# Kernel tuning notes

Measured on AMD Instinct MI355X. Metric: run time of the kernel, lower is better.

Reference implementation:

```python
import jax, jax.numpy as jnp
import numpy as np
from jax.scipy.special import logsumexp

S, L = 32768, 512  # seq_len, label_num


def setup_inputs() -> dict:
    key = jax.random.key(0)
    k1, k2, k3 = jax.random.split(key, 3)
    logit = jax.random.normal(k1, (S, L), dtype=jnp.float32)   # emissions [S, L]
    labels = jax.random.randint(k2, (S,), 0, L)                # gold path [S]
    T = jax.random.normal(k3, (L, L), dtype=jnp.float32)       # T[next, prev]
    return {"logit": logit, "labels": labels, "T": T}


def _crf_loss(logit, T, labels):
    # Forward algorithm: alpha_t[j] = logsumexp_i(alpha_{t-1}[i] + T[j, i]) + feat_t[j]
    alpha0 = logit[0]

    def step(alpha, feat):
        new_alpha = logsumexp(alpha[None, :] + T, axis=1) + feat  # [L]
        return new_alpha, None

    alpha_final, _ = jax.lax.scan(step, alpha0, logit[1:])
    log_Z = logsumexp(alpha_final)

    # Gold path score: feat_0[y0] + sum_{t>0} (feat_t[y_t] + T[y_t, y_{t-1}])
    emit = logit[0, labels[0]] + jnp.sum(logit[jnp.arange(1, logit.shape[0]), labels[1:]])
    trans = jnp.sum(T[labels[1:], labels[:-1]])
    gold = emit + trans
    return log_Z - gold


def reference(logit, labels, T):
    return _crf_loss(logit, T, labels)
```

## Files before the change

kernel.cpp:

```cpp
#include <hip/hip_runtime.h>
#include <stdint.h>


#define S_LEN 32768
#define L 512
#define CH 16
#define NCF 2048
#define WGF 128
#define WGB 128
#define LN448 6.104793232f
#define LN2   0.6931471806f

#define OFF_EAF  0
#define OFF_EAB  (256*1024)
#define OFF_G    (512*1024)
#define OFF_H    (OFF_G + 2048*512*2)
#define OFF_LSE  (OFF_H + 2048*512*2)
#define OFF_GOLD (OFF_LSE + 4104*4)

typedef float v4f __attribute__((ext_vector_type(4)));

__device__ __forceinline__ float b2f(unsigned short u){
  return __uint_as_float(((unsigned)u) << 16);
}
__device__ __forceinline__ unsigned short f2b(float x){
  unsigned u = __float_as_uint(x);
  return (unsigned short)((u + 0x7fffu + ((u >> 16) & 1u)) >> 16);
}
__device__ __forceinline__ unsigned char to_fp8(float v){
  int u = __builtin_amdgcn_cvt_pk_fp8_f32(v, v, 0, false);
  return (unsigned char)(u & 0xff);
}

extern "C" __global__ void crf_prep(const float* __restrict__ T,
                                    unsigned char* __restrict__ EAf,
                                    unsigned char* __restrict__ EAb){
  int tid = blockIdx.x*512 + threadIdx.x;
  int r    = tid & 7;
  int lane = (tid >> 3) & 63;
  int kt   = (tid >> 9) & 15;
  int mtw  = tid >> 13;
  int j = (mtw >> 2)*64 + (mtw & 3)*16 + (lane & 15);
  int i = kt*32 + ((lane >> 4) << 3) + r;
  EAf[tid] = to_fp8(2.0f * __expf(T[j*L + i]));
  EAb[tid] = to_fp8(2.0f * __expf(T[i*L + j]));
}

extern "C" __global__ __launch_bounds__(512, 2)
void crf_chunks(const float* __restrict__ logit,
                const unsigned char* __restrict__ EAf,
                const unsigned char* __restrict__ EAb,
                unsigned short* __restrict__ G, unsigned short* __restrict__ H){
  __shared__ __align__(16) unsigned char Pl[2][8192];
  __shared__ float sPart[16][8];

  const int tid  = threadIdx.x;
  const int w    = tid >> 6;
  const int lane = tid & 63;
  const int quad = lane >> 4;
  const int cl   = lane & 15;
  const bool fwd = (blockIdx.x < WGF);
  const int  b   = fwd ? blockIdx.x : (blockIdx.x - WGF);
  const int  cg  = fwd ? (b*16 + cl) : (1 + b*16 + cl);
  const int  cgc = min(cg, NCF-1);
  const bool isc0 = fwd && (cg == 0);
  const int  jrow0 = w*64 + quad*4;

  const long* EA = (const long*)(fwd ? EAf : EAb);
  long eA[4][16];
  #pragma unroll
  for (int mt = 0; mt < 4; ++mt)
    #pragma unroll
    for (int kt = 0; kt < 16; ++kt)
      eA[mt][kt] = EA[(((w<<2)+mt)<<4 | kt)*64 + lane];

  float vr[4][4];
  if (fwd) {
    #pragma unroll
    for (int mt = 0; mt < 4; ++mt)
      #pragma unroll
      for (int r = 0; r < 4; ++r) vr[mt][r] = 1.0f;
  } else {
    const int t0 = cgc*CH + CH - 1;
    const float* lp = logit + (size_t)t0*L + jrow0;
    #pragma unroll
    for (int mt = 0; mt < 4; ++mt) {
      float4 x = *(const float4*)(lp + mt*16);
      vr[mt][0] = __expf(x.x); vr[mt][1] = __expf(x.y);
      vr[mt][2] = __expf(x.z); vr[mt][3] = __expf(x.w);
    }
  }
  float m = 0.0f;
  int par = 0;

  auto renorm_store = [&](int dst){
    float mx = vr[0][0];
    #pragma unroll
    for (int mt = 0; mt < 4; ++mt)
      #pragma unroll
      for (int r = 0; r < 4; ++r) mx = fmaxf(mx, vr[mt][r]);
    mx = fmaxf(mx, __shfl_xor(mx, 16));
    mx = fmaxf(mx, __shfl_xor(mx, 32));
    if (quad == 0) sPart[cl][w] = mx;
    __syncthreads();
    float4 pa = *(const float4*)&sPart[cl][0];
    float4 pb = *(const float4*)&sPart[cl][4];
    float M = fmaxf(fmaxf(fmaxf(pa.x,pa.y),fmaxf(pa.z,pa.w)),
                    fmaxf(fmaxf(pb.x,pb.y),fmaxf(pb.z,pb.w)));
    float sc = 448.0f / M;
    #pragma unroll
    for (int mt = 0; mt < 4; ++mt) {
      int u = __builtin_amdgcn_cvt_pk_fp8_f32(vr[mt][0]*sc, vr[mt][1]*sc, 0, false);
      u     = __builtin_amdgcn_cvt_pk_fp8_f32(vr[mt][2]*sc, vr[mt][3]*sc, u, true);
      int r0 = jrow0 + mt*16;
      *(int*)&Pl[dst][(r0 >> 5)*512 + ((((r0 >> 3) & 3)*16 + cl) << 3) + (r0 & 7)] = u;
    }
    m += __logf(M) - LN448;
    __syncthreads();
  };

  renorm_store(0);

  for (int k = 0; k < CH; ++k) {
    const bool last = (k == CH-1);
    const bool useF = fwd || !last;

    v4f acc[4];
    #pragma unroll
    for (int mt = 0; mt < 4; ++mt) acc[mt] = (v4f){0.f,0.f,0.f,0.f};
    #pragma unroll
    for (int kt = 0; kt < 16; ++kt) {
      long bb = *(const long*)&Pl[par][kt*512 + lane*8];
      #pragma unroll
      for (int mt = 0; mt < 4; ++mt)
        acc[mt] = __builtin_amdgcn_mfma_f32_16x16x32_fp8_fp8(eA[mt][kt], bb, acc[mt], 0, 0, 0);
    }
    m -= LN2;

    if (useF) {
      const int t = fwd ? (cgc*CH + k) : (cgc*CH + CH - 2 - k);
      const float* lp = logit + (size_t)t*L + jrow0;
      #pragma unroll
      for (int mt = 0; mt < 4; ++mt) {
        float4 x = *(const float4*)(lp + mt*16);
        float f0 = __expf(x.x), f1 = __expf(x.y), f2 = __expf(x.z), f3 = __expf(x.w);
        vr[mt][0] = acc[mt][0]*f0; vr[mt][1] = acc[mt][1]*f1;
        vr[mt][2] = acc[mt][2]*f2; vr[mt][3] = acc[mt][3]*f3;
        if (k == 0 && isc0) {
          vr[mt][0] = f0; vr[mt][1] = f1; vr[mt][2] = f2; vr[mt][3] = f3;
        }
      }
      if (k == 0 && isc0) m = 0.0f;
    } else {
      #pragma unroll
      for (int mt = 0; mt < 4; ++mt)
        #pragma unroll
        for (int r = 0; r < 4; ++r) vr[mt][r] = acc[mt][r];
    }

    if (last) {
      if (cg <= NCF-1) {
        unsigned short* dst = (fwd ? G : H) + (size_t)cg*L + jrow0;
        #pragma unroll
        for (int mt = 0; mt < 4; ++mt) {
          ushort4 o;
          o.x = f2b(__logf(vr[mt][0]) + m); o.y = f2b(__logf(vr[mt][1]) + m);
          o.z = f2b(__logf(vr[mt][2]) + m); o.w = f2b(__logf(vr[mt][3]) + m);
          *(ushort4*)(dst + mt*16) = o;
        }
      }
    } else {
      renorm_store(par ^ 1);
      par ^= 1;
    }
  }
}

__device__ __forceinline__ float blockMax(float v, float* sred){
  #pragma unroll
  for (int off = 32; off >= 1; off >>= 1) v = fmaxf(v, __shfl_xor(v, off));
  int wid = threadIdx.x >> 6, lane = threadIdx.x & 63;
  if (lane == 0) sred[wid] = v;
  __syncthreads();
  if (threadIdx.x < 8) {
    float t = sred[threadIdx.x];
    t = fmaxf(t, __shfl_xor(t, 4));
    t = fmaxf(t, __shfl_xor(t, 2));
    t = fmaxf(t, __shfl_xor(t, 1));
    if (threadIdx.x == 0) sred[15] = t;
  }
  __syncthreads();
  float r = sred[15];
  __syncthreads();
  return r;
}
__device__ __forceinline__ float blockSum(float v, float* sred){
  #pragma unroll
  for (int off = 32; off >= 1; off >>= 1) v += __shfl_xor(v, off);
  int wid = threadIdx.x >> 6, lane = threadIdx.x & 63;
  if (lane == 0) sred[wid] = v;
  __syncthreads();
  if (threadIdx.x < 8) {
    float t = sred[threadIdx.x];
    t += __shfl_xor(t, 4); t += __shfl_xor(t, 2); t += __shfl_xor(t, 1);
    if (threadIdx.x == 0) sred[15] = t;
  }
  __syncthreads();
  float r = sred[15];
  __syncthreads();
  return r;
}

extern "C" __global__ __launch_bounds__(512)
void crf_lse(const unsigned short* __restrict__ G,
             const unsigned short* __restrict__ H,
             float* __restrict__ lsebuf){
  __shared__ float sred[16];
  int j = threadIdx.x, b = blockIdx.x;
  if (b == 0) {
    float v = b2f(G[(size_t)(NCF-1)*L + j]);
    float M = blockMax(v, sred);
    float ss = blockSum(__expf(v - M), sred);
    if (j == 0) lsebuf[2*NCF] = M + __logf(ss);
  } else {
    int c = b;
    float h = b2f(H[(size_t)c*L + j]);
    float g = b2f(G[(size_t)(c-1)*L + j]);
    float v1 = h + g;
    float M1 = blockMax(v1, sred);
    float s1 = blockSum(__expf(v1 - M1), sred);
    float M2 = blockMax(h, sred);
    float s2 = blockSum(__expf(h - M2), sred);
    if (j == 0) { lsebuf[c] = M1 + __logf(s1); lsebuf[NCF + c] = M2 + __logf(s2); }
  }
}

extern "C" __global__ void crf_gold(const float* __restrict__ logit,
                                    const int* __restrict__ labels,
                                    const float* __restrict__ T,
                                    float* __restrict__ part){
  __shared__ float sred[8];
  int tid = threadIdx.x;
  float acc = 0.f;
  for (int t = blockIdx.x*256 + tid; t < S_LEN; t += gridDim.x*256) {
    int yt = labels[t];
    float v = logit[(size_t)t*L + yt];
    if (t > 0) v += T[yt*L + labels[t-1]];
    acc += v;
  }
  #pragma unroll
  for (int off = 32; off >= 1; off >>= 1) acc += __shfl_xor(acc, off);
  int wid = tid >> 6, lane = tid & 63;
  if (lane == 0) sred[wid] = acc;
  __syncthreads();
  if (tid == 0) part[blockIdx.x] = sred[0] + sred[1] + sred[2] + sred[3];
}

extern "C" __global__ __launch_bounds__(512)
void crf_final(const float* __restrict__ lsebuf,
               const float* __restrict__ part,
               float* __restrict__ out){
  __shared__ float sred[16];
  int j = threadIdx.x;
  float acc = 0.f;
  #pragma unroll
  for (int c = j; c < NCF; c += 512)
    if (c >= 1) acc += lsebuf[c] - lsebuf[NCF + c];
  if (j < 64) acc -= part[j];
  float s = blockSum(acc, sred);
  if (j == 0) out[0] = lsebuf[2*NCF] + s;
}

extern "C" void kernel_launch(void* const* d_in, const int* in_sizes, int n_in,
                              void* d_out, int out_size, void* d_ws, size_t ws_size,
                              hipStream_t stream){
  const float* logit = (const float*)d_in[0];
  const int* labels  = (const int*)d_in[1];
  const float* T     = (const float*)d_in[2];
  float* out = (float*)d_out;
  char* ws = (char*)d_ws;
  unsigned char* EAf = (unsigned char*)(ws + OFF_EAF);
  unsigned char* EAb = (unsigned char*)(ws + OFF_EAB);
  unsigned short* G  = (unsigned short*)(ws + OFF_G);
  unsigned short* H  = (unsigned short*)(ws + OFF_H);
  float* lsebuf = (float*)(ws + OFF_LSE);
  float* part   = (float*)(ws + OFF_GOLD);

  crf_prep  <<<512, 512, 0, stream>>>(T, EAf, EAb);
  crf_chunks<<<WGF + WGB, 512, 0, stream>>>(logit, EAf, EAb, G, H);
  crf_lse   <<<NCF, 512, 0, stream>>>(G, H, lsebuf);
  crf_gold  <<<64, 256, 0, stream>>>(logit, labels, T, part);
  crf_final <<<1, 512, 0, stream>>>(lsebuf, part, out);
}
```

Before: 148.5 us.

## Fuse LSE, gold and final kernels into one tail kernel; prefetch emissions

Merges the per-chunk logsumexp, gold-path score and final reduction kernels into a single launch. The last block, found with an atomic ticket, does the final sum. The LSE work moves from one 512-thread block per chunk to one wavefront per chunk, which removes the block-wide barriers. The chunk kernel also prefetches emission rows two steps ahead into registers and computes their exponentials before the MFMA loop, to hide global load latency on the serial chain. This removes two kernel launches and a lot of synchronization, at the cost of more register pressure in the chunk kernel and reliance on a threadfence and atomic pattern.

```diff
diff --git a/kernel.cpp b/kernel.cpp
--- a/kernel.cpp
+++ b/kernel.cpp
@@ -10,13 +10,17 @@
 #define WGB 128
 #define LN448 6.104793232f
 #define LN2   0.6931471806f
+#define NB_LSE  256
+#define NB_GOLD 64
+#define NB_TAIL (NB_LSE + NB_GOLD)
 
 #define OFF_EAF  0
 #define OFF_EAB  (256*1024)
 #define OFF_G    (512*1024)
-#define OFF_H    (OFF_G + 2048*512*2)
-#define OFF_LSE  (OFF_H + 2048*512*2)
-#define OFF_GOLD (OFF_LSE + 4104*4)
+#define OFF_H    (OFF_G + NCF*L*2)
+#define OFF_LSE  (OFF_H + NCF*L*2)
+#define OFF_GOLD (OFF_LSE + 4100*4)
+#define OFF_TKT  (OFF_GOLD + 64*4)
 
 typedef float v4f __attribute__((ext_vector_type(4)));
 
@@ -34,8 +38,10 @@
 
 extern "C" __global__ void crf_prep(const float* __restrict__ T,
                                     unsigned char* __restrict__ EAf,
-                                    unsigned char* __restrict__ EAb){
+                                    unsigned char* __restrict__ EAb,
+                                    unsigned int* __restrict__ ticket){
   int tid = blockIdx.x*512 + threadIdx.x;
+  if (tid == 0) *ticket = 0;
   int r    = tid & 7;
   int lane = (tid >> 3) & 63;
   int kt   = (tid >> 9) & 15;
@@ -74,6 +80,20 @@
     for (int kt = 0; kt < 16; ++kt)
       eA[mt][kt] = EA[(((w<<2)+mt)<<4 | kt)*64 + lane];
 
+  auto t_of = [&](int k)->int {
+    if (fwd) return cgc*CH + min(k, CH-1);
+    int kk = CH - 2 - k; if (kk < 0) kk = 0;
+    return cgc*CH + kk;
+  };
+
+  float4 pf[2][4];
+  #pragma unroll
+  for (int kk = 0; kk < 2; ++kk) {
+    const float* lp = logit + (size_t)t_of(kk)*L + jrow0;
+    #pragma unroll
+    for (int mt = 0; mt < 4; ++mt) pf[kk][mt] = *(const float4*)(lp + mt*16);
+  }
+
   float vr[4][4];
   if (fwd) {
     #pragma unroll
@@ -125,6 +145,19 @@
     const bool last = (k == CH-1);
     const bool useF = fwd || !last;
 
+    float fex[4][4];
+    #pragma unroll
+    for (int mt = 0; mt < 4; ++mt) {
+      float4 x = pf[k & 1][mt];
+      fex[mt][0] = __expf(x.x); fex[mt][1] = __expf(x.y);
+      fex[mt][2] = __expf(x.z); fex[mt][3] = __expf(x.w);
+    }
+    {
+      const float* lp = logit + (size_t)t_of(k+2)*L + jrow0;
+      #pragma unroll
+      for (int mt = 0; mt < 4; ++mt) pf[k & 1][mt] = *(const float4*)(lp + mt*16);
+    }
+
     v4f acc[4];
     #pragma unroll
     for (int mt = 0; mt < 4; ++mt) acc[mt] = (v4f){0.f,0.f,0.f,0.f};
@@ -138,16 +171,13 @@
     m -= LN2;
 
     if (useF) {
-      const int t = fwd ? (cgc*CH + k) : (cgc*CH + CH - 2 - k);
-      const float* lp = logit + (size_t)t*L + jrow0;
       #pragma unroll
       for (int mt = 0; mt < 4; ++mt) {
-        float4 x = *(const float4*)(lp + mt*16);
-        float f0 = __expf(x.x), f1 = __expf(x.y), f2 = __expf(x.z), f3 = __expf(x.w);
-        vr[mt][0] = acc[mt][0]*f0; vr[mt][1] = acc[mt][1]*f1;
-        vr[mt][2] = acc[mt][2]*f2; vr[mt][3] = acc[mt][3]*f3;
+        vr[mt][0] = acc[mt][0]*fex[mt][0]; vr[mt][1] = acc[mt][1]*fex[mt][1];
+        vr[mt][2] = acc[mt][2]*fex[mt][2]; vr[mt][3] = acc[mt][3]*fex[mt][3];
         if (k == 0 && isc0) {
-          vr[mt][0] = f0; vr[mt][1] = f1; vr[mt][2] = f2; vr[mt][3] = f3;
+          vr[mt][0] = fex[mt][0]; vr[mt][1] = fex[mt][1];
+          vr[mt][2] = fex[mt][2]; vr[mt][3] = fex[mt][3];
         }
       }
       if (k == 0 && isc0) m = 0.0f;
@@ -176,24 +206,6 @@
   }
 }
 
-__device__ __forceinline__ float blockMax(float v, float* sred){
-  #pragma unroll
-  for (int off = 32; off >= 1; off >>= 1) v = fmaxf(v, __shfl_xor(v, off));
-  int wid = threadIdx.x >> 6, lane = threadIdx.x & 63;
-  if (lane == 0) sred[wid] = v;
-  __syncthreads();
-  if (threadIdx.x < 8) {
-    float t = sred[threadIdx.x];
-    t = fmaxf(t, __shfl_xor(t, 4));
-    t = fmaxf(t, __shfl_xor(t, 2));
-    t = fmaxf(t, __shfl_xor(t, 1));
-    if (threadIdx.x == 0) sred[15] = t;
-  }
-  __syncthreads();
-  float r = sred[15];
-  __syncthreads();
-  return r;
-}
 __device__ __forceinline__ float blockSum(float v, float* sred){
   #pragma unroll
   for (int off = 32; off >= 1; off >>= 1) v += __shfl_xor(v, off);
@@ -212,63 +224,87 @@
 }
 
 extern "C" __global__ __launch_bounds__(512)
-void crf_lse(const unsigned short* __restrict__ G,
-             const unsigned short* __restrict__ H,
-             float* __restrict__ lsebuf){
+void crf_tail(const float* __restrict__ logit, const int* __restrict__ labels,
+              const float* __restrict__ T,
+              const unsigned short* __restrict__ G,
+              const unsigned short* __restrict__ H,
+              float* __restrict__ lsebuf, float* __restrict__ part,
+              unsigned int* __restrict__ ticket, float* __restrict__ out){
   __shared__ float sred[16];
-  int j = threadIdx.x, b = blockIdx.x;
-  if (b == 0) {
-    float v = b2f(G[(size_t)(NCF-1)*L + j]);
-    float M = blockMax(v, sred);
-    float ss = blockSum(__expf(v - M), sred);
-    if (j == 0) lsebuf[2*NCF] = M + __logf(ss);
+  __shared__ bool amLast;
+  const int tid = threadIdx.x, lane = tid & 63, wv = tid >> 6;
+  const int b = blockIdx.x;
+
+  if (b < NB_LSE) {
+    const int task = b*8 + wv;
+    if (task == 0) {
+      const ushort4* gp = (const ushort4*)(G + (size_t)(NCF-1)*L + lane*8);
+      ushort4 u0 = gp[0], u1 = gp[1];
+      float v[8] = {b2f(u0.x),b2f(u0.y),b2f(u0.z),b2f(u0.w),
+                    b2f(u1.x),b2f(u1.y),b2f(u1.z),b2f(u1.w)};
+      float M = v[0];
+      #pragma unroll
+      for (int r = 1; r < 8; ++r) M = fmaxf(M, v[r]);
+      #pragma unroll
+      for (int off = 1; off <= 32; off <<= 1) M = fmaxf(M, __shfl_xor(M, off));
+      float s = 0.f;
+      #pragma unroll
+      for (int r = 0; r < 8; ++r) s += __expf(v[r] - M);
+      #pragma unroll
+      for (int off = 1; off <= 32; off <<= 1) s += __shfl_xor(s, off);
+      if (lane == 0) lsebuf[4096] = M + __logf(s);
+    } else {
+      const int c = task;
+      const ushort4* hp = (const ushort4*)(H + (size_t)c*L + lane*8);
+      const ushort4* gp = (const ushort4*)(G + (size_t)(c-1)*L + lane*8);
+      ushort4 h0 = hp[0], h1 = hp[1], g0 = gp[0], g1 = gp[1];
+      float hh[8] = {b2f(h0.x),b2f(h0.y),b2f(h0.z),b2f(h0.w),
+                     b2f(h1.x),b2f(h1.y),b2f(h1.z),b2f(h1.w)};
+      float aa[8] = {hh[0]+b2f(g0.x),hh[1]+b2f(g0.y),hh[2]+b2f(g0.z),hh[3]+b2f(g0.w),
+                     hh[4]+b2f(g1.x),hh[5]+b2f(g1.y),hh[6]+b2f(g1.z),hh[7]+b2f(g1.w)};
+      float Ma = aa[0], Mh = hh[0];
+      #pragma unroll
+      for (int r = 1; r < 8; ++r) { Ma = fmaxf(Ma, aa[r]); Mh = fmaxf(Mh, hh[r]); }
+      #pragma unroll
+      for (int off = 1; off <= 32; off <<= 1) {
+        Ma = fmaxf(Ma, __shfl_xor(Ma, off));
+        Mh = fmaxf(Mh, __shfl_xor(Mh, off));
+      }
+      float sa = 0.f, sh = 0.f;
+      #pragma unroll
+      for (int r = 0; r < 8; ++r) { sa += __expf(aa[r]-Ma); sh += __expf(hh[r]-Mh); }
+      #pragma unroll
+      for (int off = 1; off <= 32; off <<= 1) {
+        sa += __shfl_xor(sa, off);
+        sh += __shfl_xor(sh, off);
+      }
+      if (lane == 0) { lsebuf[c] = Ma + __logf(sa); lsebuf[2048 + c] = Mh + __logf(sh); }
+    }
   } else {
-    int c = b;
-    float h = b2f(H[(size_t)c*L + j]);
-    float g = b2f(G[(size_t)(c-1)*L + j]);
-    float v1 = h + g;
-    float M1 = blockMax(v1, sred);
-    float s1 = blockSum(__expf(v1 - M1), sred);
-    float M2 = blockMax(h, sred);
-    float s2 = blockSum(__expf(h - M2), sred);
-    if (j == 0) { lsebuf[c] = M1 + __logf(s1); lsebuf[NCF + c] = M2 + __logf(s2); }
-  }
-}
-
-extern "C" __global__ void crf_gold(const float* __restrict__ logit,
-                                    const int* __restrict__ labels,
-                                    const float* __restrict__ T,
-                                    float* __restrict__ part){
-  __shared__ float sred[8];
-  int tid = threadIdx.x;
-  float acc = 0.f;
-  for (int t = blockIdx.x*256 + tid; t < S_LEN; t += gridDim.x*256) {
+    const int t = (b - NB_LSE)*512 + tid;
     int yt = labels[t];
     float v = logit[(size_t)t*L + yt];
     if (t > 0) v += T[yt*L + labels[t-1]];
-    acc += v;
-  }
-  #pragma unroll
-  for (int off = 32; off >= 1; off >>= 1) acc += __shfl_xor(acc, off);
-  int wid = tid >> 6, lane = tid & 63;
-  if (lane == 0) sred[wid] = acc;
-  __syncthreads();
-  if (tid == 0) part[blockIdx.x] = sred[0] + sred[1] + sred[2] + sred[3];
-}
-
-extern "C" __global__ __launch_bounds__(512)
-void crf_final(const float* __restrict__ lsebuf,
-               const float* __restrict__ part,
-               float* __restrict__ out){
-  __shared__ float sred[16];
-  int j = threadIdx.x;
-  float acc = 0.f;
-  #pragma unroll
-  for (int c = j; c < NCF; c += 512)
-    if (c >= 1) acc += lsebuf[c] - lsebuf[NCF + c];
-  if (j < 64) acc -= part[j];
-  float s = blockSum(acc, sred);
-  if (j == 0) out[0] = lsebuf[2*NCF] + s;
+    float s = blockSum(v, sred);
+    if (tid == 0) part[b - NB_LSE] = s;
+  }
+
+  __syncthreads();
+  if (tid == 0) {
+    __threadfence();
+    amLast = (atomicAdd(ticket, 1u) == (unsigned)(NB_TAIL - 1));
+  }
+  __syncthreads();
+  if (amLast) {
+    __threadfence();
+    float acc = 0.f;
+    #pragma unroll
+    for (int c = tid; c < NCF; c += 512)
+      if (c >= 1) acc += lsebuf[c] - lsebuf[2048 + c];
+    if (tid < NB_GOLD) acc -= part[tid];
+    float s = blockSum(acc, sred);
+    if (tid == 0) out[0] = lsebuf[4096] + s;
+  }
 }
 
 extern "C" void kernel_launch(void* const* d_in, const int* in_sizes, int n_in,
@@ -285,10 +321,10 @@
   unsigned short* H  = (unsigned short*)(ws + OFF_H);
   float* lsebuf = (float*)(ws + OFF_LSE);
   float* part   = (float*)(ws + OFF_GOLD);
-
-  crf_prep  <<<512, 512, 0, stream>>>(T, EAf, EAb);
+  unsigned int* ticket = (unsigned int*)(ws + OFF_TKT);
+
+  crf_prep  <<<512, 512, 0, stream>>>(T, EAf, EAb, ticket);
   crf_chunks<<<WGF + WGB, 512, 0, stream>>>(logit, EAf, EAb, G, H);
-  crf_lse   <<<NCF, 512, 0, stream>>>(G, H, lsebuf);
-  crf_gold  <<<64, 256, 0, stream>>>(logit, labels, T, part);
-  crf_final <<<1, 512, 0, stream>>>(lsebuf, part, out);
-}
+  crf_tail  <<<NB_TAIL, 512, 0, stream>>>(logit, labels, T, G, H,
+                                          lsebuf, part, ticket, out);
+}
```

Result: slower. 175.0 us (+17.8%).
